# Kernel tuning notes

Measured on AMD Instinct MI355X. Metric: run time of the kernel, lower is better.

## Reference

```python
import jax, jax.numpy as jnp
import numpy as np

LN_EPS = 1e-5

def _layernorm(x, w, b):
    mu = jnp.mean(x, axis=-1, keepdims=True)
    var = jnp.mean(jnp.square(x - mu), axis=-1, keepdims=True)
    return (x - mu) * jax.lax.rsqrt(var + LN_EPS) * w + b

def setup_inputs() -> dict:
    key = jax.random.key(0)
    ks = jax.random.split(key, 8)
    B, T, C, N = 4, 4096, 1024, 64
    H = 4 * C  # mlp hidden
    x = jax.random.normal(ks[0], (B, T, C), dtype=jnp.float32)
    log_tau = jnp.zeros((N,), dtype=jnp.float32)           # log(1.0)
    log_dt = jnp.zeros((), dtype=jnp.float32)              # log(1.0)
    mix = jax.random.normal(ks[1], (C, N), dtype=jnp.float32) * 0.02
    D = jnp.ones((C,), dtype=jnp.float32)
    norm1_w = jnp.ones((C,), dtype=jnp.float32)
    norm1_b = jnp.zeros((C,), dtype=jnp.float32)
    norm2_w = jnp.ones((C,), dtype=jnp.float32)
    norm2_b = jnp.zeros((C,), dtype=jnp.float32)
    fc1_w = jax.random.normal(ks[2], (H, C), dtype=jnp.float32) * 0.02
    fc1_b = jnp.zeros((H,), dtype=jnp.float32)
    fc2_w = jax.random.normal(ks[3], (C, H), dtype=jnp.float32) * 0.02
    fc2_b = jnp.zeros((C,), dtype=jnp.float32)
    return {"x": x, "log_tau": log_tau, "log_dt": log_dt, "mix": mix, "D": D,
            "norm1_w": norm1_w, "norm1_b": norm1_b, "norm2_w": norm2_w, "norm2_b": norm2_b,
            "fc1_w": fc1_w, "fc1_b": fc1_b, "fc2_w": fc2_w, "fc2_b": fc2_b}

def _s4d(u, log_tau, log_dt, mix, D):
    # u: (B, C, T). K_c[t] = sum_j mix[c,j] * exp(-softplus(log_tau[j])*softplus(log_dt)*t)
    B, C, T = u.shape
    tau = jax.nn.softplus(log_tau)                    # (N,)
    dt = jax.nn.softplus(log_dt)                      # scalar
    t = jnp.arange(T, dtype=jnp.float32)              # (T,)
    E = jnp.exp(-(tau * dt)[:, None] * t[None, :])    # (N, T)
    # torch module computes the exponent table under no_grad (cached buffer)
    E = jax.lax.stop_gradient(E)
    K = mix @ E                                       # (C, T)
    # causal depthwise conv via FFT: y[b,c,t] = sum_{s<=t} K[c,t-s] u[b,c,s]
    n = 2 * T
    Uf = jnp.fft.rfft(u, n=n, axis=-1)                # (B, C, n//2+1)
    Kf = jnp.fft.rfft(K, n=n, axis=-1)                # (C, n//2+1)
    y = jnp.fft.irfft(Uf * Kf[None], n=n, axis=-1)[..., :T]
    return y + D[None, :, None] * u

def reference(x, log_tau, log_dt, mix, D, norm1_w, norm1_b, norm2_w, norm2_b,
              fc1_w, fc1_b, fc2_w, fc2_b):
    # x: (B, T, C)
    h = _layernorm(x, norm1_w, norm1_b)
    h2 = _s4d(jnp.swapaxes(h, 1, 2), log_tau, log_dt, mix, D)  # (B, C, T)
    x = x + jnp.swapaxes(h2, 1, 2)                    # alpha_s4 = 1.0
    g = _layernorm(x, norm2_w, norm2_b)
    g = jax.nn.gelu(g @ fc1_w.T + fc1_b, approximate=False)
    g = g @ fc2_w.T + fc2_b
    return x + g                                      # alpha_mlp = 1.0
```

## Files before the change

kernel.cpp:

```cpp
#include <hip/hip_runtime.h>
#include <math.h>

typedef __attribute__((ext_vector_type(8))) short bf16x8;
typedef __attribute__((ext_vector_type(4))) float f32x4;

__device__ __forceinline__ unsigned short f2bf(float f) {
  union { float f; unsigned u; } v; v.f = f;
  unsigned r = v.u + 0x7fff + ((v.u >> 16) & 1);
  return (unsigned short)(r >> 16);
}

__device__ __forceinline__ float bf2f(unsigned short h) {
  union { unsigned u; float f; } v; v.u = ((unsigned)h) << 16;
  return v.f;
}

__device__ __forceinline__ void gll16(const void* g, void* l) {
  __builtin_amdgcn_global_load_lds(
      (const __attribute__((address_space(1))) void*)g,
      (__attribute__((address_space(3))) void*)l, 16, 0, 0);
}

#define BB 4
#define TT 4096
#define CC 1024
#define HH 4096
#define MM 16384

__global__ __launch_bounds__(256) void ln_f32_kernel(
    const float* __restrict__ x, const float* __restrict__ w,
    const float* __restrict__ b, float* __restrict__ out)
{
  size_t row = blockIdx.x;
  const float4* xr = (const float4*)(x + row * CC);
  int tid = threadIdx.x;
  float4 v = xr[tid];
  float s = v.x + v.y + v.z + v.w;
  float sq = v.x*v.x + v.y*v.y + v.z*v.z + v.w*v.w;
  for (int o = 32; o; o >>= 1) { s += __shfl_xor(s, o); sq += __shfl_xor(sq, o); }
  __shared__ float ss[4], ssq[4];
  int wv = tid >> 6, lane = tid & 63;
  if (lane == 0) { ss[wv] = s; ssq[wv] = sq; }
  __syncthreads();
  s = ss[0] + ss[1] + ss[2] + ss[3];
  sq = ssq[0] + ssq[1] + ssq[2] + ssq[3];
  float mu = s * (1.f / CC);
  float var = sq * (1.f / CC) - mu * mu;
  float rstd = rsqrtf(var + 1e-5f);
  float4 wv4 = ((const float4*)w)[tid];
  float4 bv4 = ((const float4*)b)[tid];
  float4 o;
  o.x = (v.x - mu) * rstd * wv4.x + bv4.x;
  o.y = (v.y - mu) * rstd * wv4.y + bv4.y;
  o.z = (v.z - mu) * rstd * wv4.z + bv4.z;
  o.w = (v.w - mu) * rstd * wv4.w + bv4.w;
  ((float4*)(out + row * CC))[tid] = o;
}

__global__ __launch_bounds__(256) void ln_bf16_kernel(
    const float* __restrict__ x, const float* __restrict__ w,
    const float* __restrict__ b, unsigned short* __restrict__ out)
{
  size_t row = blockIdx.x;
  const float4* xr = (const float4*)(x + row * CC);
  int tid = threadIdx.x;
  float4 v = xr[tid];
  float s = v.x + v.y + v.z + v.w;
  float sq = v.x*v.x + v.y*v.y + v.z*v.z + v.w*v.w;
  for (int o = 32; o; o >>= 1) { s += __shfl_xor(s, o); sq += __shfl_xor(sq, o); }
  __shared__ float ss[4], ssq[4];
  int wv = tid >> 6, lane = tid & 63;
  if (lane == 0) { ss[wv] = s; ssq[wv] = sq; }
  __syncthreads();
  s = ss[0] + ss[1] + ss[2] + ss[3];
  sq = ssq[0] + ssq[1] + ssq[2] + ssq[3];
  float mu = s * (1.f / CC);
  float var = sq * (1.f / CC) - mu * mu;
  float rstd = rsqrtf(var + 1e-5f);
  float4 wv4 = ((const float4*)w)[tid];
  float4 bv4 = ((const float4*)b)[tid];
  ushort4 o;
  o.x = f2bf((v.x - mu) * rstd * wv4.x + bv4.x);
  o.y = f2bf((v.y - mu) * rstd * wv4.y + bv4.y);
  o.z = f2bf((v.z - mu) * rstd * wv4.z + bv4.z);
  o.w = f2bf((v.w - mu) * rstd * wv4.w + bv4.w);
  ((ushort4*)(out + row * CC))[tid] = o;
}

__global__ __launch_bounds__(256) void transpose_kernel(
    const float* __restrict__ in, float* __restrict__ out)
{
  __shared__ float tile[64][65];
  size_t boff = (size_t)blockIdx.z * TT * CC;
  int r0 = blockIdx.y * 64;
  int c0 = blockIdx.x * 64;
  int tid = threadIdx.x;
#pragma unroll
  for (int i = 0; i < 16; ++i) {
    int idx = tid + i * 256;
    int r = idx >> 6, cx = idx & 63;
    tile[r][cx] = in[boff + (size_t)(r0 + r) * CC + c0 + cx];
  }
  __syncthreads();
#pragma unroll
  for (int i = 0; i < 16; ++i) {
    int idx = tid + i * 256;
    int r = idx >> 6, cx = idx & 63;
    out[boff + (size_t)(c0 + r) * TT + r0 + cx] = tile[cx][r];
  }
}

__global__ __launch_bounds__(256) void transadd_kernel(
    const float* __restrict__ y, const float* __restrict__ x,
    float* __restrict__ x2)
{
  __shared__ float tile[64][65];
  size_t boff = (size_t)blockIdx.z * TT * CC;
  int t0 = blockIdx.x * 64;
  int c0 = blockIdx.y * 64;
  int tid = threadIdx.x;
#pragma unroll
  for (int i = 0; i < 16; ++i) {
    int idx = tid + i * 256;
    int r = idx >> 6, cx = idx & 63;
    tile[r][cx] = y[boff + (size_t)(c0 + r) * TT + t0 + cx];
  }
  __syncthreads();
#pragma unroll
  for (int i = 0; i < 16; ++i) {
    int idx = tid + i * 256;
    int r = idx >> 6, cx = idx & 63;
    size_t off = boff + (size_t)(t0 + r) * CC + c0 + cx;
    x2[off] = x[off] + tile[cx][r];
  }
}

#define SWZ(row, byteoff) (((row) << 7) + ((byteoff) ^ (((row) & 7) << 4)))

__global__ __launch_bounds__(256) void s4d_kernel(
    const float* __restrict__ hT,
    const float* __restrict__ log_tau,
    const float* __restrict__ log_dt,
    const float* __restrict__ mix,
    const float* __restrict__ Dv,
    float* __restrict__ y)
{
  int bc = blockIdx.x;
  int c = bc & (CC - 1);
  int tid = threadIdx.x;
  int lane = tid & 63, w = tid >> 6;
  int m = lane & 15, g = lane >> 4;

  __shared__ unsigned short s_uh[64 * 64], s_ul[64 * 64];
  __shared__ unsigned short s_A2[64 * 64], s_Ac[64 * 64];
  __shared__ unsigned short s_T[64 * 64], s_Wt[64 * 64];
  __shared__ float s_P[64 * 64];
  __shared__ float s_a[64], s_rL[64], s_mix[64], s_K[64], s_Kp[4 * 64];

  const float4* urow = (const float4*)(hT + (size_t)bc * TT);
#pragma unroll
  for (int q = 0; q < 4; ++q) {
    int i = tid + q * 256;
    float4 v = urow[i];
    int row = i >> 4;
    int colb = (i & 15) * 8;
    float f[4] = {v.x, v.y, v.z, v.w};
    ushort4 hh, ll;
    unsigned short* hp = (unsigned short*)&hh;
    unsigned short* lp = (unsigned short*)&ll;
#pragma unroll
    for (int r = 0; r < 4; ++r) {
      unsigned short hb = f2bf(f[r]);
      hp[r] = hb;
      lp[r] = f2bf(f[r] - bf2f(hb));
    }
    *(ushort4*)((char*)s_uh + SWZ(row, colb)) = hh;
    *(ushort4*)((char*)s_ul + SWZ(row, colb)) = ll;
  }
  if (tid < 64) {
    float lt = log_tau[tid];
    float tau = (lt > 20.f) ? lt : log1pf(expf(lt));
    float ld = log_dt[0];
    float dt = (ld > 20.f) ? ld : log1pf(expf(ld));
    float a = tau * dt;
    s_a[tid] = a;
    s_rL[tid] = expf(-64.f * a);
    s_mix[tid] = mix[c * 64 + tid];
  }
  __syncthreads();

#pragma unroll
  for (int e = 0; e < 16; ++e) {
    int idx = tid + e * 256;
    int rA = idx >> 6, cA = idx & 63;
    s_A2[SWZ(rA, cA * 2) >> 1] = f2bf(expf(-s_a[rA] * (float)(63 - cA)));
    s_Ac[SWZ(rA, cA * 2) >> 1] = f2bf(expf(-s_a[cA] * (float)(rA + 1)));
  }
  __syncthreads();

  {
    int d = tid & 63, q = tid >> 6;
    float p = 0.f;
    if (d == 0) {
#pragma unroll
      for (int j = 16 * q; j < 16 * q + 16; ++j) p += s_mix[j];
    } else {
#pragma unroll
      for (int j = 16 * q; j < 16 * q + 16; ++j)
        p = fmaf(s_mix[j], bf2f(s_Ac[SWZ(d - 1, j * 2) >> 1]), p);
    }
    s_Kp[q * 64 + d] = p;
  }

  {
    f32x4 accP[4] = {};
    bf16x8 a2f[2];
#pragma unroll
    for (int ks = 0; ks < 2; ++ks)
      a2f[ks] = *(const bf16x8*)((const char*)s_A2 + SWZ(16 * w + m, ks * 64 + g * 16));
#pragma unroll
    for (int ct = 0; ct < 4; ++ct) {
#pragma unroll
      for (int ks = 0; ks < 2; ++ks) {
        bf16x8 bh = *(const bf16x8*)((const char*)s_uh + SWZ(ct * 16 + m, ks * 64 + g * 16));
        bf16x8 bl = *(const bf16x8*)((const char*)s_ul + SWZ(ct * 16 + m, ks * 64 + g * 16));
        accP[ct] = __builtin_amdgcn_mfma_f32_16x16x32_bf16(a2f[ks], bh, accP[ct], 0, 0, 0);
        accP[ct] = __builtin_amdgcn_mfma_f32_16x16x32_bf16(a2f[ks], bl, accP[ct], 0, 0, 0);
      }
    }
#pragma unroll
    for (int ct = 0; ct < 4; ++ct)
      *(f32x4*)&s_P[(ct * 16 + m) * 64 + 16 * w + g * 4] = accP[ct];
  }
  __syncthreads();

  if (tid < 64)
    s_K[tid] = s_Kp[tid] + s_Kp[64 + tid] + s_Kp[128 + tid] + s_Kp[192 + tid];
  __syncthreads();

#pragma unroll
  for (int e = 0; e < 16; ++e) {
    int idx = tid + e * 256;
    int t = idx >> 6, s = idx & 63;
    float val = (s <= t) ? s_K[t - s] : 0.f;
    s_T[SWZ(t, s * 2) >> 1] = f2bf(val);
  }
  if (tid < 64) {
    int j = tid;
    float S = 0.f, rL = s_rL[j], mj = s_mix[j];
    for (int k = 0; k < 64; ++k) {
      s_Wt[SWZ(k, j * 2) >> 1] = f2bf(mj * S);
      S = fmaf(rL, S, s_P[k * 64 + j]);
    }
  }
  __syncthreads();

  f32x4 accY[4] = {};
  {
    bf16x8 acf[2], tf[2];
#pragma unroll
    for (int ks = 0; ks < 2; ++ks) {
      acf[ks] = *(const bf16x8*)((const char*)s_Ac + SWZ(16 * w + m, ks * 64 + g * 16));
      tf[ks]  = *(const bf16x8*)((const char*)s_T  + SWZ(16 * w + m, ks * 64 + g * 16));
    }
#pragma unroll
    for (int ct = 0; ct < 4; ++ct) {
#pragma unroll
      for (int ks = 0; ks < 2; ++ks) {
        bf16x8 bw  = *(const bf16x8*)((const char*)s_Wt + SWZ(ct * 16 + m, ks * 64 + g * 16));
        bf16x8 uhf = *(const bf16x8*)((const char*)s_uh + SWZ(ct * 16 + m, ks * 64 + g * 16));
        bf16x8 ulf = *(const bf16x8*)((const char*)s_ul + SWZ(ct * 16 + m, ks * 64 + g * 16));
        accY[ct] = __builtin_amdgcn_mfma_f32_16x16x32_bf16(acf[ks], bw,  accY[ct], 0, 0, 0);
        accY[ct] = __builtin_amdgcn_mfma_f32_16x16x32_bf16(tf[ks],  uhf, accY[ct], 0, 0, 0);
        accY[ct] = __builtin_amdgcn_mfma_f32_16x16x32_bf16(tf[ks],  ulf, accY[ct], 0, 0, 0);
      }
    }
  }

  float Dc = Dv[c];
  float* yrow = y + (size_t)bc * TT;
#pragma unroll
  for (int ct = 0; ct < 4; ++ct) {
    int k = ct * 16 + m;
    int t0 = 16 * w + g * 4;
    float4 o;
    float* op = (float*)&o;
#pragma unroll
    for (int r = 0; r < 4; ++r) {
      int t = t0 + r;
      float uf = bf2f(s_uh[SWZ(k, t * 2) >> 1]) + bf2f(s_ul[SWZ(k, t * 2) >> 1]);
      op[r] = accY[ct][r] + Dc * uf;
    }
    *(float4*)(yrow + k * 64 + t0) = o;
  }
}

__global__ __launch_bounds__(256) void cvt_bf16_kernel(
    const float* __restrict__ in, unsigned short* __restrict__ out)
{
  int i = blockIdx.x * 256 + threadIdx.x;
  float4 v = ((const float4*)in)[i];
  ushort4 o;
  o.x = f2bf(v.x); o.y = f2bf(v.y); o.z = f2bf(v.z); o.w = f2bf(v.w);
  ((ushort4*)out)[i] = o;
}

__global__ __launch_bounds__(256) void gemm_gelu_kernel(
    const unsigned short* __restrict__ A, int lda,
    const unsigned short* __restrict__ Bw, int ldb,
    const float* __restrict__ bias, unsigned short* __restrict__ Out, int ldo,
    int K, int NB, int cpx)
{
  __shared__ unsigned short sA[128 * 32];
  __shared__ unsigned short sB[128 * 32];
  int id = blockIdx.x;
  int swz = (id & 7) * cpx + (id >> 3);
  int m0 = (swz / NB) * 128, n0 = (swz % NB) * 128;
  int tid = threadIdx.x, lane = tid & 63, wv = tid >> 6;
  int wm = wv >> 1, wn = wv & 1;

  f32x4 acc[4][4] = {};

  int idx0 = tid, idx1 = tid + 256;
  int r0 = idx0 >> 2, cg0 = (idx0 & 3) * 8;
  int r1 = idx1 >> 2, cg1 = (idx1 & 3) * 8;
  const unsigned short* Ab = A + (size_t)m0 * lda;
  const unsigned short* Bb = Bw + (size_t)n0 * ldb;

  int arow = wm * 64 + (lane & 15);
  int brow = wn * 64 + (lane & 15);
  int kk = (lane >> 4) * 8;

  for (int k0 = 0; k0 < K; k0 += 32) {
    gll16(Ab + (size_t)r0 * lda + k0 + cg0, sA + idx0 * 8);
    gll16(Ab + (size_t)r1 * lda + k0 + cg1, sA + idx1 * 8);
    gll16(Bb + (size_t)r0 * ldb + k0 + cg0, sB + idx0 * 8);
    gll16(Bb + (size_t)r1 * ldb + k0 + cg1, sB + idx1 * 8);
    __syncthreads();
    bf16x8 af[4], bfr[4];
#pragma unroll
    for (int mi = 0; mi < 4; ++mi)
      af[mi] = *(const bf16x8*)(sA + (arow + mi * 16) * 32 + kk);
#pragma unroll
    for (int ni = 0; ni < 4; ++ni)
      bfr[ni] = *(const bf16x8*)(sB + (brow + ni * 16) * 32 + kk);
#pragma unroll
    for (int mi = 0; mi < 4; ++mi)
#pragma unroll
      for (int ni = 0; ni < 4; ++ni)
        acc[mi][ni] = __builtin_amdgcn_mfma_f32_16x16x32_bf16(af[mi], bfr[ni], acc[mi][ni], 0, 0, 0);
    __syncthreads();
  }

#pragma unroll
  for (int mi = 0; mi < 4; ++mi) {
    int rbase = m0 + wm * 64 + mi * 16 + (lane >> 4) * 4;
#pragma unroll
    for (int ni = 0; ni < 4; ++ni) {
      int col = n0 + wn * 64 + ni * 16 + (lane & 15);
      float bcol = bias[col];
#pragma unroll
      for (int r = 0; r < 4; ++r) {
        float v = acc[mi][ni][r] + bcol;
        v = 0.5f * v * (1.f + erff(v * 0.70710678118f));
        Out[(size_t)(rbase + r) * ldo + col] = f2bf(v);
      }
    }
  }
}

__global__ __launch_bounds__(256) void gemm_acc_kernel(
    const unsigned short* __restrict__ A, int lda,
    const unsigned short* __restrict__ Bw, int ldb,
    const float* __restrict__ bias,
    const float* add, float* Out, int K, int NB, int cpx)
{
  __shared__ unsigned short sA[128 * 32];
  __shared__ unsigned short sB[128 * 32];
  int id = blockIdx.x;
  int swz = (id & 7) * cpx + (id >> 3);
  int m0 = (swz / NB) * 128, n0 = (swz % NB) * 128;
  int tid = threadIdx.x, lane = tid & 63, wv = tid >> 6;
  int wm = wv >> 1, wn = wv & 1;

  f32x4 acc[4][4] = {};

  int idx0 = tid, idx1 = tid + 256;
  int r0 = idx0 >> 2, cg0 = (idx0 & 3) * 8;
  int r1 = idx1 >> 2, cg1 = (idx1 & 3) * 8;
  const unsigned short* Ab = A + (size_t)m0 * lda;
  const unsigned short* Bb = Bw + (size_t)n0 * ldb;

  int arow = wm * 64 + (lane & 15);
  int brow = wn * 64 + (lane & 15);
  int kk = (lane >> 4) * 8;

  for (int k0 = 0; k0 < K; k0 += 32) {
    gll16(Ab + (size_t)r0 * lda + k0 + cg0, sA + idx0 * 8);
    gll16(Ab + (size_t)r1 * lda + k0 + cg1, sA + idx1 * 8);
    gll16(Bb + (size_t)r0 * ldb + k0 + cg0, sB + idx0 * 8);
    gll16(Bb + (size_t)r1 * ldb + k0 + cg1, sB + idx1 * 8);
    __syncthreads();
    bf16x8 af[4], bfr[4];
#pragma unroll
    for (int mi = 0; mi < 4; ++mi)
      af[mi] = *(const bf16x8*)(sA + (arow + mi * 16) * 32 + kk);
#pragma unroll
    for (int ni = 0; ni < 4; ++ni)
      bfr[ni] = *(const bf16x8*)(sB + (brow + ni * 16) * 32 + kk);
#pragma unroll
    for (int mi = 0; mi < 4; ++mi)
#pragma unroll
      for (int ni = 0; ni < 4; ++ni)
        acc[mi][ni] = __builtin_amdgcn_mfma_f32_16x16x32_bf16(af[mi], bfr[ni], acc[mi][ni], 0, 0, 0);
    __syncthreads();
  }

#pragma unroll
  for (int mi = 0; mi < 4; ++mi) {
    int rbase = m0 + wm * 64 + mi * 16 + (lane >> 4) * 4;
#pragma unroll
    for (int ni = 0; ni < 4; ++ni) {
      int col = n0 + wn * 64 + ni * 16 + (lane & 15);
      float bcol = bias ? bias[col] : 0.f;
#pragma unroll
      for (int r = 0; r < 4; ++r) {
        size_t off = (size_t)(rbase + r) * CC + col;
        Out[off] = acc[mi][ni][r] + bcol + add[off];
      }
    }
  }
}

extern "C" void kernel_launch(void* const* d_in, const int* in_sizes, int n_in,
                              void* d_out, int out_size, void* d_ws, size_t ws_size,
                              hipStream_t stream)
{
  const float* x       = (const float*)d_in[0];
  const float* log_tau = (const float*)d_in[1];
  const float* log_dt  = (const float*)d_in[2];
  const float* mix     = (const float*)d_in[3];
  const float* Dv      = (const float*)d_in[4];
  const float* n1w     = (const float*)d_in[5];
  const float* n1b     = (const float*)d_in[6];
  const float* n2w     = (const float*)d_in[7];
  const float* n2b     = (const float*)d_in[8];
  const float* w1      = (const float*)d_in[9];
  const float* b1      = (const float*)d_in[10];
  const float* w2      = (const float*)d_in[11];
  const float* b2      = (const float*)d_in[12];

  char* ws = (char*)d_ws;
  float* buf0 = (float*)ws;
  float* buf1 = (float*)(ws + (64ull << 20));
  unsigned short* a2  = (unsigned short*)(ws + (128ull << 20));
  unsigned short* w1b = (unsigned short*)(ws + (160ull << 20));
  unsigned short* w2b = (unsigned short*)(ws + (168ull << 20));
  unsigned short* act = (unsigned short*)buf0;
  float* out = (float*)d_out;

  ln_f32_kernel<<<MM, 256, 0, stream>>>(x, n1w, n1b, buf0);
  transpose_kernel<<<dim3(CC / 64, TT / 64, BB), 256, 0, stream>>>(buf0, buf1);
  s4d_kernel<<<BB * CC, 256, 0, stream>>>(buf1, log_tau, log_dt, mix, Dv, buf0);
  transadd_kernel<<<dim3(TT / 64, CC / 64, BB), 256, 0, stream>>>(buf0, x, buf1);
  ln_bf16_kernel<<<MM, 256, 0, stream>>>(buf1, n2w, n2b, a2);
  cvt_bf16_kernel<<<(HH * CC / 4) / 256, 256, 0, stream>>>(w1, w1b);
  cvt_bf16_kernel<<<(HH * CC / 4) / 256, 256, 0, stream>>>(w2, w2b);

  gemm_gelu_kernel<<<2048, 256, 0, stream>>>(
      a2, CC, w1b, CC, b1, act, 2048, CC, 16, 256);
  gemm_acc_kernel<<<1024, 256, 0, stream>>>(
      act, 2048, w2b, HH, b2, buf1, out, 2048, 8, 128);
  gemm_gelu_kernel<<<2048, 256, 0, stream>>>(
      a2, CC, w1b + (size_t)2048 * CC, CC, b1 + 2048, act, 2048, CC, 16, 256);
  gemm_acc_kernel<<<1024, 256, 0, stream>>>(
      act, 2048, w2b + 2048, HH, (const float*)nullptr, out, out, 2048, 8, 128);
}
```

Measured before the change: 830.9 us.

## Double-buffer LDS tiles in both MLP GEMM kernels to overlap loads with MFMA

Both GEMM kernels (fc1+GELU and fc2+residual) now use two LDS buffers per operand. The next K-slice is issued via global_load_lds into the alternate buffer before the current slice's MFMAs run, and one barrier per iteration replaces two. This is meant to hide global-to-LDS latency behind compute. It doubles LDS use per block, which may lower occupancy, and the compiler may still insert conservative vmcnt waits before the LDS reads, which would limit the overlap.

```diff
diff --git a/kernel.cpp b/kernel.cpp
--- a/kernel.cpp
+++ b/kernel.cpp
@@ -311,8 +311,8 @@
     const float* __restrict__ bias, unsigned short* __restrict__ Out, int ldo,
     int K, int NB, int cpx)
 {
-  __shared__ unsigned short sA[128 * 32];
-  __shared__ unsigned short sB[128 * 32];
+  __shared__ unsigned short sA[2][128 * 32];
+  __shared__ unsigned short sB[2][128 * 32];
   int id = blockIdx.x;
   int swz = (id & 7) * cpx + (id >> 3);
   int m0 = (swz / NB) * 128, n0 = (swz % NB) * 128;
@@ -331,25 +331,39 @@
   int brow = wn * 64 + (lane & 15);
   int kk = (lane >> 4) * 8;
 
-  for (int k0 = 0; k0 < K; k0 += 32) {
-    gll16(Ab + (size_t)r0 * lda + k0 + cg0, sA + idx0 * 8);
-    gll16(Ab + (size_t)r1 * lda + k0 + cg1, sA + idx1 * 8);
-    gll16(Bb + (size_t)r0 * ldb + k0 + cg0, sB + idx0 * 8);
-    gll16(Bb + (size_t)r1 * ldb + k0 + cg1, sB + idx1 * 8);
-    __syncthreads();
+  int nt = K >> 5;
+  gll16(Ab + (size_t)r0 * lda + cg0, sA[0] + idx0 * 8);
+  gll16(Ab + (size_t)r1 * lda + cg1, sA[0] + idx1 * 8);
+  gll16(Bb + (size_t)r0 * ldb + cg0, sB[0] + idx0 * 8);
+  gll16(Bb + (size_t)r1 * ldb + cg1, sB[0] + idx1 * 8);
+  __syncthreads();
+
+  int cur = 0;
+  for (int t = 0; t < nt; ++t) {
+    if (t + 1 < nt) {
+      int kn = (t + 1) << 5;
+      gll16(Ab + (size_t)r0 * lda + kn + cg0, sA[cur ^ 1] + idx0 * 8);
+      gll16(Ab + (size_t)r1 * lda + kn + cg1, sA[cur ^ 1] + idx1 * 8);
+      gll16(Bb + (size_t)r0 * ldb + kn + cg0, sB[cur ^ 1] + idx0 * 8);
+      gll16(Bb + (size_t)r1 * ldb + kn + cg1, sB[cur ^ 1] + idx1 * 8);
+    }
+    __builtin_amdgcn_sched_barrier(0);
+    const unsigned short* sAc = sA[cur];
+    const unsigned short* sBc = sB[cur];
     bf16x8 af[4], bfr[4];
 #pragma unroll
     for (int mi = 0; mi < 4; ++mi)
-      af[mi] = *(const bf16x8*)(sA + (arow + mi * 16) * 32 + kk);
+      af[mi] = *(const bf16x8*)(sAc + (arow + mi * 16) * 32 + kk);
 #pragma unroll
     for (int ni = 0; ni < 4; ++ni)
-      bfr[ni] = *(const bf16x8*)(sB + (brow + ni * 16) * 32 + kk);
+      bfr[ni] = *(const bf16x8*)(sBc + (brow + ni * 16) * 32 + kk);
 #pragma unroll
     for (int mi = 0; mi < 4; ++mi)
 #pragma unroll
       for (int ni = 0; ni < 4; ++ni)
         acc[mi][ni] = __builtin_amdgcn_mfma_f32_16x16x32_bf16(af[mi], bfr[ni], acc[mi][ni], 0, 0, 0);
     __syncthreads();
+    cur ^= 1;
   }
 
 #pragma unroll
@@ -375,8 +389,8 @@
     const float* __restrict__ bias,
     const float* add, float* Out, int K, int NB, int cpx)
 {
-  __shared__ unsigned short sA[128 * 32];
-  __shared__ unsigned short sB[128 * 32];
+  __shared__ unsigned short sA[2][128 * 32];
+  __shared__ unsigned short sB[2][128 * 32];
   int id = blockIdx.x;
   int swz = (id & 7) * cpx + (id >> 3);
   int m0 = (swz / NB) * 128, n0 = (swz % NB) * 128;
@@ -395,25 +409,39 @@
   int brow = wn * 64 + (lane & 15);
   int kk = (lane >> 4) * 8;
 
-  for (int k0 = 0; k0 < K; k0 += 32) {
-    gll16(Ab + (size_t)r0 * lda + k0 + cg0, sA + idx0 * 8);
-    gll16(Ab + (size_t)r1 * lda + k0 + cg1, sA + idx1 * 8);
-    gll16(Bb + (size_t)r0 * ldb + k0 + cg0, sB + idx0 * 8);
-    gll16(Bb + (size_t)r1 * ldb + k0 + cg1, sB + idx1 * 8);
-    __syncthreads();
+  int nt = K >> 5;
+  gll16(Ab + (size_t)r0 * lda + cg0, sA[0] + idx0 * 8);
+  gll16(Ab + (size_t)r1 * lda + cg1, sA[0] + idx1 * 8);
+  gll16(Bb + (size_t)r0 * ldb + cg0, sB[0] + idx0 * 8);
+  gll16(Bb + (size_t)r1 * ldb + cg1, sB[0] + idx1 * 8);
+  __syncthreads();
+
+  int cur = 0;
+  for (int t = 0; t < nt; ++t) {
+    if (t + 1 < nt) {
+      int kn = (t + 1) << 5;
+      gll16(Ab + (size_t)r0 * lda + kn + cg0, sA[cur ^ 1] + idx0 * 8);
+      gll16(Ab + (size_t)r1 * lda + kn + cg1, sA[cur ^ 1] + idx1 * 8);
+      gll16(Bb + (size_t)r0 * ldb + kn + cg0, sB[cur ^ 1] + idx0 * 8);
+      gll16(Bb + (size_t)r1 * ldb + kn + cg1, sB[cur ^ 1] + idx1 * 8);
+    }
+    __builtin_amdgcn_sched_barrier(0);
+    const unsigned short* sAc = sA[cur];
+    const unsigned short* sBc = sB[cur];
     bf16x8 af[4], bfr[4];
 #pragma unroll
     for (int mi = 0; mi < 4; ++mi)
-      af[mi] = *(const bf16x8*)(sA + (arow + mi * 16) * 32 + kk);
+      af[mi] = *(const bf16x8*)(sAc + (arow + mi * 16) * 32 + kk);
 #pragma unroll
     for (int ni = 0; ni < 4; ++ni)
-      bfr[ni] = *(const bf16x8*)(sB + (brow + ni * 16) * 32 + kk);
+      bfr[ni] = *(const bf16x8*)(sBc + (brow + ni * 16) * 32 + kk);
 #pragma unroll
     for (int mi = 0; mi < 4; ++mi)
 #pragma unroll
       for (int ni = 0; ni < 4; ++ni)
         acc[mi][ni] = __builtin_amdgcn_mfma_f32_16x16x32_bf16(af[mi], bfr[ni], acc[mi][ni], 0, 0, 0);
     __syncthreads();
+    cur ^= 1;
   }
 
 #pragma unroll
```

New measurement: 813.5 us. -2.1%, faster.

## Rewrite MLP GEMMs with 256x256 tiles, double-buffered swizzled LDS, 512 threads

Applied to the files above, without the earlier changes.

Both MLP GEMM kernels move from 128x128 tiles with K-step 32 and single-buffered LDS to 256x256 tiles with K-step 64, 8 waves per block, XOR-swizzled LDS layout and a two-stage global_load_lds prefetch pipeline driven by manual vmcnt waits and barriers. MFMA sections are wrapped in s_setprio. The aim is more data reuse per loaded tile, fewer LDS bank conflicts, and overlap of global loads with MFMA work. The cost is higher register and LDS pressure (128KB LDS per block with two blocks requested per CU) and fewer blocks, which may cause spills or low occupancy.

```diff
diff --git a/kernel.cpp b/kernel.cpp
--- a/kernel.cpp
+++ b/kernel.cpp
@@ -26,6 +26,8 @@
 #define CC 1024
 #define HH 4096
 #define MM 16384
+
+#define SWZ(row, byteoff) (((row) << 7) + ((byteoff) ^ (((row) & 7) << 4)))
 
 __global__ __launch_bounds__(256) void ln_f32_kernel(
     const float* __restrict__ x, const float* __restrict__ w,
@@ -135,8 +137,6 @@
   }
 }
 
-#define SWZ(row, byteoff) (((row) << 7) + ((byteoff) ^ (((row) & 7) << 4)))
-
 __global__ __launch_bounds__(256) void s4d_kernel(
     const float* __restrict__ hT,
     const float* __restrict__ log_tau,
@@ -305,127 +305,134 @@
   ((ushort4*)out)[i] = o;
 }
 
-__global__ __launch_bounds__(256) void gemm_gelu_kernel(
+
+#define GEMM256_BODY(A_, lda_, B_, ldb_, K_)                                   \
+  __shared__ unsigned short sA[2][256 * 64];                                   \
+  __shared__ unsigned short sB[2][256 * 64];                                   \
+  int id = blockIdx.x;                                                         \
+  int swz = (id & 7) * cpx + (id >> 3);                                        \
+  int m0 = (swz / NB) * 256, n0 = (swz % NB) * 256;                            \
+  int tid = threadIdx.x, lane = tid & 63;                                      \
+  int wid = tid >> 6, wm = wid >> 2, wn = wid & 3;                             \
+  int m = lane & 15, g = lane >> 4;                                            \
+  const unsigned short* aSrc[4];                                               \
+  const unsigned short* bSrc[4];                                               \
+  int ldsOff[4];                                                               \
+  _Pragma("unroll")                                                            \
+  for (int i = 0; i < 4; ++i) {                                                \
+    int j = i * 512 + tid;                                                     \
+    int row = j >> 3;                                                          \
+    int colb = ((j & 7) * 16) ^ ((row & 7) << 4);                              \
+    aSrc[i] = (A_) + (size_t)(m0 + row) * (lda_) + (colb >> 1);                \
+    bSrc[i] = (B_) + (size_t)(n0 + row) * (ldb_) + (colb >> 1);                \
+    ldsOff[i] = j * 8;                                                         \
+  }                                                                            \
+  f32x4 acc[8][4] = {};                                                        \
+  int nt = (K_) >> 6;                                                          \
+                                                \
+  _Pragma("unroll")                                                            \
+  for (int i = 0; i < 4; ++i) gll16(aSrc[i], &sA[0][ldsOff[i]]);               \
+  _Pragma("unroll")                                                            \
+  for (int i = 0; i < 4; ++i) gll16(bSrc[i], &sB[0][ldsOff[i]]);               \
+  _Pragma("unroll")                                                            \
+  for (int i = 0; i < 4; ++i) gll16(aSrc[i] + 64, &sA[1][ldsOff[i]]);          \
+  _Pragma("unroll")                                                            \
+  for (int i = 0; i < 4; ++i) gll16(bSrc[i] + 64, &sB[1][ldsOff[i]]);          \
+  asm volatile("s_waitcnt vmcnt(8)" ::: "memory");                             \
+  asm volatile("s_barrier" ::: "memory");                                      \
+  int cur = 0;                                                                 \
+  for (int kt = 0; kt < nt; ++kt) {                                            \
+    const unsigned short* sAc = sA[cur];                                       \
+    const unsigned short* sBc = sB[cur];                                       \
+    bf16x8 bfr[4][2];                                                          \
+    _Pragma("unroll")                                                          \
+    for (int ni = 0; ni < 4; ++ni)                                             \
+      _Pragma("unroll")                                                        \
+      for (int ks = 0; ks < 2; ++ks)                                           \
+        bfr[ni][ks] = *(const bf16x8*)((const char*)sBc +                      \
+                        SWZ(wn * 64 + ni * 16 + m, ks * 64 + g * 16));         \
+    _Pragma("unroll")                                                          \
+    for (int q = 0; q < 4; ++q) {                                              \
+      bf16x8 af[2][2];                                                         \
+      _Pragma("unroll")                                                        \
+      for (int mi = 0; mi < 2; ++mi)                                           \
+        _Pragma("unroll")                                                      \
+        for (int ks = 0; ks < 2; ++ks)                                         \
+          af[mi][ks] = *(const bf16x8*)((const char*)sAc +                     \
+                         SWZ(wm * 128 + (q * 2 + mi) * 16 + m,                 \
+                             ks * 64 + g * 16));                               \
+      __builtin_amdgcn_s_setprio(1);                                           \
+      _Pragma("unroll")                                                        \
+      for (int mi = 0; mi < 2; ++mi)                                           \
+        _Pragma("unroll")                                                      \
+        for (int ni = 0; ni < 4; ++ni) {                                       \
+          acc[q * 2 + mi][ni] = __builtin_amdgcn_mfma_f32_16x16x32_bf16(       \
+              af[mi][0], bfr[ni][0], acc[q * 2 + mi][ni], 0, 0, 0);            \
+          acc[q * 2 + mi][ni] = __builtin_amdgcn_mfma_f32_16x16x32_bf16(       \
+              af[mi][1], bfr[ni][1], acc[q * 2 + mi][ni], 0, 0, 0);            \
+        }                                                                      \
+      __builtin_amdgcn_s_setprio(0);                                           \
+    }                                                                          \
+    if (kt + 1 < nt) {                                                         \
+      asm volatile("s_barrier" ::: "memory");   \
+      if (kt + 2 < nt) {                                                       \
+        int ko = (kt + 2) << 6;                                                \
+        _Pragma("unroll")                                                      \
+        for (int i = 0; i < 4; ++i) gll16(aSrc[i] + ko, &sA[cur][ldsOff[i]]);  \
+        _Pragma("unroll")                                                      \
+        for (int i = 0; i < 4; ++i) gll16(bSrc[i] + ko, &sB[cur][ldsOff[i]]);  \
+        asm volatile("s_waitcnt vmcnt(8)" ::: "memory");                       \
+      } else {                                                                 \
+        asm volatile("s_waitcnt vmcnt(0)" ::: "memory");                       \
+      }                                                                        \
+      asm volatile("s_barrier" ::: "memory");   \
+      cur ^= 1;                                                                \
+    }                                                                          \
+  }
+
+__global__ __launch_bounds__(512, 2) void gemm_gelu_kernel(
     const unsigned short* __restrict__ A, int lda,
     const unsigned short* __restrict__ Bw, int ldb,
     const float* __restrict__ bias, unsigned short* __restrict__ Out, int ldo,
     int K, int NB, int cpx)
 {
-  __shared__ unsigned short sA[128 * 32];
-  __shared__ unsigned short sB[128 * 32];
-  int id = blockIdx.x;
-  int swz = (id & 7) * cpx + (id >> 3);
-  int m0 = (swz / NB) * 128, n0 = (swz % NB) * 128;
-  int tid = threadIdx.x, lane = tid & 63, wv = tid >> 6;
-  int wm = wv >> 1, wn = wv & 1;
-
-  f32x4 acc[4][4] = {};
-
-  int idx0 = tid, idx1 = tid + 256;
-  int r0 = idx0 >> 2, cg0 = (idx0 & 3) * 8;
-  int r1 = idx1 >> 2, cg1 = (idx1 & 3) * 8;
-  const unsigned short* Ab = A + (size_t)m0 * lda;
-  const unsigned short* Bb = Bw + (size_t)n0 * ldb;
-
-  int arow = wm * 64 + (lane & 15);
-  int brow = wn * 64 + (lane & 15);
-  int kk = (lane >> 4) * 8;
-
-  for (int k0 = 0; k0 < K; k0 += 32) {
-    gll16(Ab + (size_t)r0 * lda + k0 + cg0, sA + idx0 * 8);
-    gll16(Ab + (size_t)r1 * lda + k0 + cg1, sA + idx1 * 8);
-    gll16(Bb + (size_t)r0 * ldb + k0 + cg0, sB + idx0 * 8);
-    gll16(Bb + (size_t)r1 * ldb + k0 + cg1, sB + idx1 * 8);
-    __syncthreads();
-    bf16x8 af[4], bfr[4];
-#pragma unroll
-    for (int mi = 0; mi < 4; ++mi)
-      af[mi] = *(const bf16x8*)(sA + (arow + mi * 16) * 32 + kk);
-#pragma unroll
-    for (int ni = 0; ni < 4; ++ni)
-      bfr[ni] = *(const bf16x8*)(sB + (brow + ni * 16) * 32 + kk);
-#pragma unroll
-    for (int mi = 0; mi < 4; ++mi)
-#pragma unroll
-      for (int ni = 0; ni < 4; ++ni)
-        acc[mi][ni] = __builtin_amdgcn_mfma_f32_16x16x32_bf16(af[mi], bfr[ni], acc[mi][ni], 0, 0, 0);
-    __syncthreads();
-  }
-
-#pragma unroll
-  for (int mi = 0; mi < 4; ++mi) {
-    int rbase = m0 + wm * 64 + mi * 16 + (lane >> 4) * 4;
+  GEMM256_BODY(A, lda, Bw, ldb, K)
+
+#pragma unroll
+  for (int mi = 0; mi < 8; ++mi) {
+    int row = m0 + wm * 128 + mi * 16 + g * 4;
 #pragma unroll
     for (int ni = 0; ni < 4; ++ni) {
-      int col = n0 + wn * 64 + ni * 16 + (lane & 15);
+      int col = n0 + wn * 64 + ni * 16 + m;
       float bcol = bias[col];
 #pragma unroll
       for (int r = 0; r < 4; ++r) {
         float v = acc[mi][ni][r] + bcol;
         v = 0.5f * v * (1.f + erff(v * 0.70710678118f));
-        Out[(size_t)(rbase + r) * ldo + col] = f2bf(v);
+        Out[(size_t)(row + r) * ldo + col] = f2bf(v);
       }
     }
   }
 }
 
-__global__ __launch_bounds__(256) void gemm_acc_kernel(
+__global__ __launch_bounds__(512, 2) void gemm_acc_kernel(
     const unsigned short* __restrict__ A, int lda,
     const unsigned short* __restrict__ Bw, int ldb,
     const float* __restrict__ bias,
     const float* add, float* Out, int K, int NB, int cpx)
 {
-  __shared__ unsigned short sA[128 * 32];
-  __shared__ unsigned short sB[128 * 32];
-  int id = blockIdx.x;
-  int swz = (id & 7) * cpx + (id >> 3);
-  int m0 = (swz / NB) * 128, n0 = (swz % NB) * 128;
-  int tid = threadIdx.x, lane = tid & 63, wv = tid >> 6;
-  int wm = wv >> 1, wn = wv & 1;
-
-  f32x4 acc[4][4] = {};
-
-  int idx0 = tid, idx1 = tid + 256;
-  int r0 = idx0 >> 2, cg0 = (idx0 & 3) * 8;
-  int r1 = idx1 >> 2, cg1 = (idx1 & 3) * 8;
-  const unsigned short* Ab = A + (size_t)m0 * lda;
-  const unsigned short* Bb = Bw + (size_t)n0 * ldb;
-
-  int arow = wm * 64 + (lane & 15);
-  int brow = wn * 64 + (lane & 15);
-  int kk = (lane >> 4) * 8;
-
-  for (int k0 = 0; k0 < K; k0 += 32) {
-    gll16(Ab + (size_t)r0 * lda + k0 + cg0, sA + idx0 * 8);
-    gll16(Ab + (size_t)r1 * lda + k0 + cg1, sA + idx1 * 8);
-    gll16(Bb + (size_t)r0 * ldb + k0 + cg0, sB + idx0 * 8);
-    gll16(Bb + (size_t)r1 * ldb + k0 + cg1, sB + idx1 * 8);
-    __syncthreads();
-    bf16x8 af[4], bfr[4];
-#pragma unroll
-    for (int mi = 0; mi < 4; ++mi)
-      af[mi] = *(const bf16x8*)(sA + (arow + mi * 16) * 32 + kk);
-#pragma unroll
-    for (int ni = 0; ni < 4; ++ni)
-      bfr[ni] = *(const bf16x8*)(sB + (brow + ni * 16) * 32 + kk);
-#pragma unroll
-    for (int mi = 0; mi < 4; ++mi)
-#pragma unroll
-      for (int ni = 0; ni < 4; ++ni)
-        acc[mi][ni] = __builtin_amdgcn_mfma_f32_16x16x32_bf16(af[mi], bfr[ni], acc[mi][ni], 0, 0, 0);
-    __syncthreads();
-  }
-
-#pragma unroll
-  for (int mi = 0; mi < 4; ++mi) {
-    int rbase = m0 + wm * 64 + mi * 16 + (lane >> 4) * 4;
+  GEMM256_BODY(A, lda, Bw, ldb, K)
+
+#pragma unroll
+  for (int mi = 0; mi < 8; ++mi) {
+    int row = m0 + wm * 128 + mi * 16 + g * 4;
 #pragma unroll
     for (int ni = 0; ni < 4; ++ni) {
-      int col = n0 + wn * 64 + ni * 16 + (lane & 15);
+      int col = n0 + wn * 64 + ni * 16 + m;
       float bcol = bias ? bias[col] : 0.f;
 #pragma unroll
       for (int r = 0; r < 4; ++r) {
-        size_t off = (size_t)(rbase + r) * CC + col;
+        size_t off = (size_t)(row + r) * CC + col;
         Out[off] = acc[mi][ni][r] + bcol + add[off];
       }
     }
@@ -467,12 +474,12 @@
   cvt_bf16_kernel<<<(HH * CC / 4) / 256, 256, 0, stream>>>(w1, w1b);
   cvt_bf16_kernel<<<(HH * CC / 4) / 256, 256, 0, stream>>>(w2, w2b);
 
-  gemm_gelu_kernel<<<2048, 256, 0, stream>>>(
-      a2, CC, w1b, CC, b1, act, 2048, CC, 16, 256);
-  gemm_acc_kernel<<<1024, 256, 0, stream>>>(
-      act, 2048, w2b, HH, b2, buf1, out, 2048, 8, 128);
-  gemm_gelu_kernel<<<2048, 256, 0, stream>>>(
-      a2, CC, w1b + (size_t)2048 * CC, CC, b1 + 2048, act, 2048, CC, 16, 256);
-  gemm_acc_kernel<<<1024, 256, 0, stream>>>(
-      act, 2048, w2b + 2048, HH, (const float*)nullptr, out, out, 2048, 8, 128);
-}
+  gemm_gelu_kernel<<<512, 512, 0, stream>>>(
+      a2, CC, w1b, CC, b1, act, 2048, CC, 8, 64);
+  gemm_acc_kernel<<<256, 512, 0, stream>>>(
+      act, 2048, w2b, HH, b2, buf1, out, 2048, 4, 32);
+  gemm_gelu_kernel<<<512, 512, 0, stream>>>(
+      a2, CC, w1b + (size_t)2048 * CC, CC, b1 + 2048, act, 2048, CC, 8, 64);
+  gemm_acc_kernel<<<256, 512, 0, stream>>>(
+      act, 2048, w2b + 2048, HH, (const float*)nullptr, out, out, 2048, 4, 32);
+}
```

Result: faster. 747.0 us (-10.1%).
